# Kernel tuning notes

Measured on AMD Instinct MI355X. Metric: run time of the kernel, lower is better.

The kernel has to match this reference:

```python
import jax, jax.numpy as jnp
import numpy as np

C = 384  # model channels

def generate_path(duration, mask):
    # duration: [B, Tp] int; mask: [B, Tp, Tf] float -> 0/1 path [B, Tp, Tf]
    cum = jnp.cumsum(duration, axis=-1)                     # [B, Tp]
    frames = jnp.arange(mask.shape[-1])                     # [Tf]
    path = (frames[None, None, :] < cum[:, :, None]).astype(mask.dtype)
    path = path - jnp.pad(path, ((0, 0), (1, 0), (0, 0)))[:, :-1]
    return path * mask


def setup_inputs() -> dict:
    key = jax.random.key(0)
    ks = jax.random.split(key, 16)
    B, Tp, Tf = 32, 512, 2048
    s = 1.0 / np.sqrt(C)
    inp = {
        "x": jax.random.normal(ks[0], (B, C, Tp), jnp.float32),
        "phone_mask": jnp.ones((B, 1, Tp), jnp.float32),
        "frame_mask": jnp.ones((B, 1, Tf), jnp.float32),
        "duration": jax.random.randint(ks[1], (B, 1, Tp), 0, 4, jnp.int32),
        "log_cf0": jax.random.normal(ks[2], (B, 1, Tf), jnp.float32),
        "vuv": jax.random.uniform(ks[3], (B, 1, Tf), jnp.float32),
        "energy": jax.random.normal(ks[4], (B, 1, Tf), jnp.float32),
        # learned params (1x1 conv == per-timestep linear)
        "dur_w": jax.random.normal(ks[5], (1, C), jnp.float32) * s,
        "dur_b": jnp.zeros((1,), jnp.float32),
        "pitch_w": jax.random.normal(ks[6], (2, C), jnp.float32) * s,
        "pitch_b": jnp.zeros((2,), jnp.float32),
        "pemb_w": jax.random.normal(ks[7], (C, 1), jnp.float32),
        "pemb_b": jnp.zeros((C,), jnp.float32),
        "enp_w": jax.random.normal(ks[8], (1, C), jnp.float32) * s,
        "enp_b": jnp.zeros((1,), jnp.float32),
        "eemb_w": jax.random.normal(ks[9], (C, 1), jnp.float32),
        "eemb_b": jnp.zeros((C,), jnp.float32),
    }
    return inp


def reference(x, phone_mask, frame_mask, duration, log_cf0, vuv, energy,
              dur_w, dur_b, pitch_w, pitch_b, pemb_w, pemb_b,
              enp_w, enp_b, eemb_w, eemb_b):
    # duration predictor (masked 1x1 conv): [B,1,Tp]
    log_duration_pred = (jnp.einsum('bct,oc->bot', x, dur_w) + dur_b[None, :, None]) * phone_mask

    # path_mask [B,Tp,Tf] = phone_mask (x) frame_mask
    path_mask = phone_mask[:, 0, :, None] * frame_mask[:, 0, None, :]
    attn_path = generate_path(duration[:, 0, :], path_mask)        # [B,Tp,Tf]

    # length regulation: [B,C,Tp] @ [B,Tp,Tf] -> [B,C,Tf]
    xf = jnp.einsum('bcp,bpf->bcf', x, attn_path.astype(x.dtype))

    # pitch predictor -> split channels into log_cf0_pred / vuv_pred
    pv = (jnp.einsum('bct,oc->bot', xf, pitch_w) + pitch_b[None, :, None]) * frame_mask
    log_cf0_pred, vuv_pred = pv[:, 0:1], pv[:, 1:2]

    # masked pitch embedding add: 1 -> C projection of ground-truth log_cf0
    pitch_emb = (jnp.einsum('bit,ci->bct', log_cf0, pemb_w) + pemb_b[None, :, None]) * frame_mask

    # energy predictor + masked energy embedding
    energy_pred = (jnp.einsum('bct,oc->bot', xf, enp_w) + enp_b[None, :, None]) * frame_mask
    energy_emb = (jnp.einsum('bit,ci->bct', energy, eemb_w) + eemb_b[None, :, None]) * frame_mask

    out = xf + pitch_emb + energy_emb
    return (out, log_duration_pred, log_cf0_pred, vuv_pred, energy_pred)
```

## Files before the change

### kernel.cpp

```cpp
#include <hip/hip_runtime.h>

#define BB 32
#define CC 384
#define TP 512
#define TF 2048

__device__ __forceinline__ int imax(int a, int b) { return a > b ? a : b; }
__device__ __forceinline__ int imin(int a, int b) { return a < b ? a : b; }

__global__ __launch_bounds__(256, 4) void mono_kernel(
    const float* __restrict__ x, const float* __restrict__ phone_mask,
    const float* __restrict__ frame_mask, const int* __restrict__ duration,
    const float* __restrict__ log_cf0, const float* __restrict__ energy,
    const float* __restrict__ dur_w, const float* __restrict__ dur_b,
    const float* __restrict__ pitch_w, const float* __restrict__ pitch_b,
    const float* __restrict__ pemb_w, const float* __restrict__ pemb_b,
    const float* __restrict__ enp_w, const float* __restrict__ enp_b,
    const float* __restrict__ eemb_w, const float* __restrict__ eemb_b,
    float* __restrict__ out, float* __restrict__ ldp, float* __restrict__ lcp,
    float* __restrict__ vup, float* __restrict__ epp) {
    int b = blockIdx.y;
    int j = blockIdx.x;
    int tid = threadIdx.x;
    int lane = tid & 63;
    int wv = tid >> 6;
    const float* xb = x + (size_t)b * CC * TP;

    if (j < 24) {
        __shared__ short po16[TF];
        __shared__ int ps[256];
        __shared__ float pm_s[TP];
        int c0 = __builtin_amdgcn_readfirstlane(j * 16);

        const float* fm_b = frame_mask + (size_t)b * TF;
        const float* lc_b = log_cf0 + (size_t)b * TF;
        const float* en_b = energy + (size_t)b * TF;
        float fmv[8], lcv[8], env[8];
#pragma unroll
        for (int q = 0; q < 8; ++q) {
            int f = q * 256 + tid;
            fmv[q] = fm_b[f];
            lcv[q] = lc_b[f];
            env[q] = en_b[f];
        }
        pm_s[tid] = phone_mask[b * TP + tid];
        pm_s[tid + 256] = phone_mask[b * TP + tid + 256];

        int2 d01 = *(const int2*)(duration + b * TP + 2 * tid);
        int d0 = d01.x, d1 = d01.y;
        ps[tid] = d0 + d1;
#pragma unroll
        for (int h = 0; h < 4; ++h) ((int*)po16)[tid + 256 * h] = -1;
        __syncthreads();
        for (int off = 1; off < 256; off <<= 1) {
            int v = (tid >= off) ? ps[tid - off] : 0;
            __syncthreads();
            ps[tid] += v;
            __syncthreads();
        }
        int excl = tid ? ps[tid - 1] : 0;
        int e0 = imin(excl + d0, TF);
        int e1 = imin(excl + d0 + d1, TF);
        for (int f = imin(excl, TF); f < e0; ++f) po16[f] = (short)(2 * tid);
        for (int f = e0; f < e1; ++f) po16[f] = (short)(2 * tid + 1);
        __syncthreads();

        int pcl[8];
        float xm[8];
#pragma unroll
        for (int q = 0; q < 8; ++q) {
            int f = q * 256 + tid;
            int p = po16[f];
            int pc = imax(p, 0);
            pcl[q] = pc;
            xm[q] = (p >= 0 ? pm_s[pc] : 0.f) * fmv[q];
        }

        float wA[16], wB[16], wC[16];
#pragma unroll
        for (int r = 0; r < 16; ++r) {
            wA[r] = pemb_w[c0 + r];
            wB[r] = pemb_b[c0 + r] + eemb_b[c0 + r];
            wC[r] = eemb_w[c0 + r];
        }
        float* ob = out + ((size_t)b * CC + c0) * TF;

#pragma unroll
        for (int r = 0; r < 16; ++r) {
            const float* xr = xb + (size_t)(c0 + r) * TP;
            float* obr = ob + (size_t)r * TF + tid;
            float sA = wA[r], sB = wB[r], sC = wC[r];
#pragma unroll
            for (int q = 0; q < 8; ++q) {
                float xv = xr[pcl[q]];
                float t = __builtin_fmaf(lcv[q], sA, sB);
                t = __builtin_fmaf(env[q], sC, t);
                float o = __builtin_fmaf(xv, xm[q], t * fmv[q]);
                __builtin_nontemporal_store(o, obr + q * 256);
            }
        }
    } else {
        int jj = j - 24;
        __shared__ float r[16 * 64];
        __shared__ int ps[256];
        __shared__ float y_lds[3 * 64];
        __shared__ float pm_lds[64];
        __shared__ short po_win[192];
        int t = jj * 64 + lane;
        float a0 = 0.f, a1 = 0.f, a2 = 0.f, a3 = 0.f;
#pragma unroll 8
        for (int i = 0; i < CC / 4; ++i) {
            int c = __builtin_amdgcn_readfirstlane(wv + 4 * i);
            float xv = xb[c * TP + t];
            a0 += xv * pitch_w[c];
            a1 += xv * pitch_w[CC + c];
            a2 += xv * enp_w[c];
            a3 += xv * dur_w[c];
        }
        r[(0 * 4 + wv) * 64 + lane] = a0;
        r[(1 * 4 + wv) * 64 + lane] = a1;
        r[(2 * 4 + wv) * 64 + lane] = a2;
        r[(3 * 4 + wv) * 64 + lane] = a3;
        int2 d01 = *(const int2*)(duration + b * TP + 2 * tid);
        int d0 = d01.x, d1 = d01.y;
        ps[tid] = d0 + d1;
        if (tid < 64) pm_lds[tid] = phone_mask[b * TP + jj * 64 + tid];
        __syncthreads();
        for (int off = 1; off < 256; off <<= 1) {
            int v = (tid >= off) ? ps[tid - off] : 0;
            __syncthreads();
            ps[tid] += v;
            __syncthreads();
        }
        float a = 0.f;
#pragma unroll
        for (int k = 0; k < 4; ++k) a += r[(wv * 4 + k) * 64 + lane];
        if (wv == 3)
            ldp[b * TP + t] = (a + dur_b[0]) * pm_lds[lane];
        else
            y_lds[wv * 64 + lane] = a;
        int base_lo = (jj > 0) ? imin(ps[jj * 32 - 1], TF) : 0;
        int base_hi = imin(ps[(jj + 1) * 32 - 1], TF);
        if (tid >= jj * 32 && tid < (jj + 1) * 32) {
            int excl = tid ? ps[tid - 1] : 0;
            int e0 = imin(excl + d0, TF);
            int e1 = imin(excl + d0 + d1, TF);
            for (int f = imin(excl, TF); f < e0; ++f) po_win[f - base_lo] = (short)(2 * tid - jj * 64);
            for (int f = e0; f < e1; ++f) po_win[f - base_lo] = (short)(2 * tid + 1 - jj * 64);
        }
        int total = imin(ps[255], TF);
        __syncthreads();
        int win = base_hi - base_lo;
        for (int idx = tid; idx < win; idx += 256) {
            int f = base_lo + idx;
            int p = po_win[idx];
            float fm = frame_mask[b * TF + f];
            float xm = pm_lds[p] * fm;
            lcp[b * TF + f] = (y_lds[p] * xm + pitch_b[0]) * fm;
            vup[b * TF + f] = (y_lds[64 + p] * xm + pitch_b[1]) * fm;
            epp[b * TF + f] = (y_lds[128 + p] * xm + enp_b[0]) * fm;
        }
        if (jj == 7) {
            for (int f = total + tid; f < TF; f += 256) {
                float fm = frame_mask[b * TF + f];
                lcp[b * TF + f] = pitch_b[0] * fm;
                vup[b * TF + f] = pitch_b[1] * fm;
                epp[b * TF + f] = enp_b[0] * fm;
            }
        }
    }
}

extern "C" void kernel_launch(void* const* d_in, const int* in_sizes, int n_in,
                              void* d_out, int out_size, void* d_ws, size_t ws_size,
                              hipStream_t stream) {
    const float* x          = (const float*)d_in[0];
    const float* phone_mask = (const float*)d_in[1];
    const float* frame_mask = (const float*)d_in[2];
    const int*   duration   = (const int*)d_in[3];
    const float* log_cf0    = (const float*)d_in[4];
    const float* energy     = (const float*)d_in[6];
    const float* dur_w      = (const float*)d_in[7];
    const float* dur_b      = (const float*)d_in[8];
    const float* pitch_w    = (const float*)d_in[9];
    const float* pitch_b    = (const float*)d_in[10];
    const float* pemb_w     = (const float*)d_in[11];
    const float* pemb_b     = (const float*)d_in[12];
    const float* enp_w      = (const float*)d_in[13];
    const float* enp_b      = (const float*)d_in[14];
    const float* eemb_w     = (const float*)d_in[15];
    const float* eemb_b     = (const float*)d_in[16];

    float* out = (float*)d_out;
    float* ldp = out + (size_t)BB * CC * TF;
    float* lcp = ldp + (size_t)BB * TP;
    float* vup = lcp + (size_t)BB * TF;
    float* epp = vup + (size_t)BB * TF;

    mono_kernel<<<dim3(32, BB), dim3(256), 0, stream>>>(
        x, phone_mask, frame_mask, duration, log_cf0, energy, dur_w, dur_b,
        pitch_w, pitch_b, pemb_w, pemb_b, enp_w, enp_b, eemb_w, eemb_b,
        out, ldp, lcp, vup, epp);
}
```

Baseline: 29.58 us.

## Use wavefront shuffle scan and float4 vectorized frame loads/stores

Replaces the barrier-heavy LDS Hillis-Steele prefix sum over durations with a per-wavefront shuffle scan plus a small cross-wave combine, removing about 16 block barriers in both branches. The expansion branch also changes its frame-to-thread mapping so each thread owns 4 consecutive frames, which allows float4 loads of the mask and feature rows, short4 LDS reads of the phone index, and 16-byte nontemporal stores of the output. The gather of x at the phone index stays scalar, and the wider per-thread stride may change LDS bank behaviour.

```diff
diff --git a/kernel.cpp b/kernel.cpp
--- a/kernel.cpp
+++ b/kernel.cpp
@@ -4,6 +4,8 @@
 #define CC 384
 #define TP 512
 #define TF 2048
+
+typedef float f32x4 __attribute__((ext_vector_type(4)));
 
 __device__ __forceinline__ int imax(int a, int b) { return a > b ? a : b; }
 __device__ __forceinline__ int imin(int a, int b) { return a < b ? a : b; }
@@ -28,8 +30,8 @@
 
     if (j < 24) {
         __shared__ short po16[TF];
-        __shared__ int ps[256];
         __shared__ float pm_s[TP];
+        __shared__ int wsum[4];
         int c0 = __builtin_amdgcn_readfirstlane(j * 16);
 
         const float* fm_b = frame_mask + (size_t)b * TF;
@@ -37,28 +39,36 @@
         const float* en_b = energy + (size_t)b * TF;
         float fmv[8], lcv[8], env[8];
 #pragma unroll
-        for (int q = 0; q < 8; ++q) {
-            int f = q * 256 + tid;
-            fmv[q] = fm_b[f];
-            lcv[q] = lc_b[f];
-            env[q] = en_b[f];
+        for (int q = 0; q < 2; ++q) {
+            int f = q * 1024 + 4 * tid;
+            float4 fm4 = *(const float4*)(fm_b + f);
+            float4 lc4 = *(const float4*)(lc_b + f);
+            float4 en4 = *(const float4*)(en_b + f);
+            fmv[4 * q + 0] = fm4.x; fmv[4 * q + 1] = fm4.y; fmv[4 * q + 2] = fm4.z; fmv[4 * q + 3] = fm4.w;
+            lcv[4 * q + 0] = lc4.x; lcv[4 * q + 1] = lc4.y; lcv[4 * q + 2] = lc4.z; lcv[4 * q + 3] = lc4.w;
+            env[4 * q + 0] = en4.x; env[4 * q + 1] = en4.y; env[4 * q + 2] = en4.z; env[4 * q + 3] = en4.w;
         }
         pm_s[tid] = phone_mask[b * TP + tid];
         pm_s[tid + 256] = phone_mask[b * TP + tid + 256];
-
         int2 d01 = *(const int2*)(duration + b * TP + 2 * tid);
         int d0 = d01.x, d1 = d01.y;
-        ps[tid] = d0 + d1;
 #pragma unroll
         for (int h = 0; h < 4; ++h) ((int*)po16)[tid + 256 * h] = -1;
-        __syncthreads();
-        for (int off = 1; off < 256; off <<= 1) {
-            int v = (tid >= off) ? ps[tid - off] : 0;
-            __syncthreads();
-            ps[tid] += v;
-            __syncthreads();
-        }
-        int excl = tid ? ps[tid - 1] : 0;
+
+        int s = d0 + d1;
+        int v = s;
+#pragma unroll
+        for (int off = 1; off < 64; off <<= 1) {
+            int t = __shfl_up(v, off, 64);
+            if (lane >= off) v += t;
+        }
+        if (lane == 63) wsum[wv] = v;
+        __syncthreads();
+        int base = 0;
+#pragma unroll
+        for (int w = 0; w < 4; ++w) base += (w < wv) ? wsum[w] : 0;
+        int excl = base + v - s;
+
         int e0 = imin(excl + d0, TF);
         int e1 = imin(excl + d0 + d1, TF);
         for (int f = imin(excl, TF); f < e0; ++f) po16[f] = (short)(2 * tid);
@@ -68,12 +78,16 @@
         int pcl[8];
         float xm[8];
 #pragma unroll
-        for (int q = 0; q < 8; ++q) {
-            int f = q * 256 + tid;
-            int p = po16[f];
-            int pc = imax(p, 0);
-            pcl[q] = pc;
-            xm[q] = (p >= 0 ? pm_s[pc] : 0.f) * fmv[q];
+        for (int q = 0; q < 2; ++q) {
+            short4 p4 = *(const short4*)(po16 + q * 1024 + 4 * tid);
+            short pk[4] = {p4.x, p4.y, p4.z, p4.w};
+#pragma unroll
+            for (int k = 0; k < 4; ++k) {
+                int p = pk[k];
+                int pc = imax(p, 0);
+                pcl[4 * q + k] = pc;
+                xm[4 * q + k] = (p >= 0 ? pm_s[pc] : 0.f) * fmv[4 * q + k];
+            }
         }
 
         float wA[16], wB[16], wC[16];
@@ -88,15 +102,20 @@
 #pragma unroll
         for (int r = 0; r < 16; ++r) {
             const float* xr = xb + (size_t)(c0 + r) * TP;
-            float* obr = ob + (size_t)r * TF + tid;
+            float* obr = ob + (size_t)r * TF;
             float sA = wA[r], sB = wB[r], sC = wC[r];
 #pragma unroll
-            for (int q = 0; q < 8; ++q) {
-                float xv = xr[pcl[q]];
-                float t = __builtin_fmaf(lcv[q], sA, sB);
-                t = __builtin_fmaf(env[q], sC, t);
-                float o = __builtin_fmaf(xv, xm[q], t * fmv[q]);
-                __builtin_nontemporal_store(o, obr + q * 256);
+            for (int q = 0; q < 2; ++q) {
+                f32x4 o;
+#pragma unroll
+                for (int k = 0; k < 4; ++k) {
+                    int i = 4 * q + k;
+                    float xv = xr[pcl[i]];
+                    float t = __builtin_fmaf(lcv[i], sA, sB);
+                    t = __builtin_fmaf(env[i], sC, t);
+                    o[k] = __builtin_fmaf(xv, xm[i], t * fmv[i]);
+                }
+                __builtin_nontemporal_store(o, (f32x4*)(obr + q * 1024 + 4 * tid));
             }
         }
     } else {
@@ -106,6 +125,7 @@
         __shared__ float y_lds[3 * 64];
         __shared__ float pm_lds[64];
         __shared__ short po_win[192];
+        __shared__ int wsumg[4];
         int t = jj * 64 + lane;
         float a0 = 0.f, a1 = 0.f, a2 = 0.f, a3 = 0.f;
 #pragma unroll 8
@@ -123,15 +143,23 @@
         r[(3 * 4 + wv) * 64 + lane] = a3;
         int2 d01 = *(const int2*)(duration + b * TP + 2 * tid);
         int d0 = d01.x, d1 = d01.y;
-        ps[tid] = d0 + d1;
         if (tid < 64) pm_lds[tid] = phone_mask[b * TP + jj * 64 + tid];
-        __syncthreads();
-        for (int off = 1; off < 256; off <<= 1) {
-            int v = (tid >= off) ? ps[tid - off] : 0;
-            __syncthreads();
-            ps[tid] += v;
-            __syncthreads();
-        }
+
+        int s = d0 + d1;
+        int v = s;
+#pragma unroll
+        for (int off = 1; off < 64; off <<= 1) {
+            int tt = __shfl_up(v, off, 64);
+            if (lane >= off) v += tt;
+        }
+        if (lane == 63) wsumg[wv] = v;
+        __syncthreads();
+        int base = 0;
+#pragma unroll
+        for (int w = 0; w < 4; ++w) base += (w < wv) ? wsumg[w] : 0;
+        ps[tid] = base + v;
+        __syncthreads();
+
         float a = 0.f;
 #pragma unroll
         for (int k = 0; k < 4; ++k) a += r[(wv * 4 + k) * 64 + lane];
```

Measured after the change: 29.17 us, median of 2. Within noise of the previous version (-1.4%).
